# Kernel optimization log

Measured on AMD Instinct MI355X. Metric: run time of the kernel, lower is better.

Reference implementation:

```python
import jax, jax.numpy as jnp
import numpy as np

H = 3        # num heads
K_ = 16      # codebook size per head (k_**H == k == 4096)
D = 768      # full vector dim
DH = D // H  # per-head dim


def setup_inputs() -> dict:
    key = jax.random.key(0)
    kx, kk, ka = jax.random.split(key, 3)
    x = jax.random.normal(kx, (16, 4096, D), dtype=jnp.float32)
    kernel = jax.random.normal(kk, (H, K_, DH), dtype=jnp.float32)
    alpha = jax.random.uniform(ka, (), dtype=jnp.float32)
    return {"x": x, "kernel": kernel, "alpha": alpha}


def reference(x, kernel, alpha):
    B, S, _ = x.shape
    xh = x.reshape(B, S, H, DH)  # split into per-head chunks
    # squared L2 distance [B,S,H,K_]; argmin identical to argmin of tf.norm
    sq = (jnp.sum(xh * xh, axis=-1)[..., None]
          - 2.0 * jnp.einsum('bshd,hkd->bshk', xh, kernel)
          + jnp.sum(kernel * kernel, axis=-1))
    ind = jnp.argmin(sq, axis=-1)              # [B,S,H] int
    v = kernel[jnp.arange(H), ind]             # per-head gather -> [B,S,H,DH]
    v = v.reshape(B, S, D)
    out = alpha * x + (1.0 - alpha) * v        # convex blend
    base = (K_ ** jnp.arange(H)).astype(ind.dtype)  # [1, K_, K_^2]
    code = jnp.sum(ind * base, axis=-1)        # packed code [B,S]
    return out, code
```

## Files before the change

### kernel.cpp

```cpp
#include <hip/hip_runtime.h>


#define NH 3
#define NK 16
#define DHEAD 256
#define DFULL 768
#define TB 4
#define BLK 256

typedef float f2 __attribute__((ext_vector_type(2)));
typedef float f4 __attribute__((ext_vector_type(4)));

__device__ __forceinline__ float dpp_xor1(float x) {
    return __builtin_bit_cast(float, __builtin_amdgcn_mov_dpp(
        __builtin_bit_cast(int, x), 0xB1, 0xF, 0xF, false));
}
__device__ __forceinline__ float dpp_xor2(float x) {
    return __builtin_bit_cast(float, __builtin_amdgcn_mov_dpp(
        __builtin_bit_cast(int, x), 0x4E, 0xF, 0xF, false));
}
__device__ __forceinline__ float swz_xor4(float x) {
    return __builtin_bit_cast(float, __builtin_amdgcn_ds_swizzle(
        __builtin_bit_cast(int, x), 0x101F));
}
__device__ __forceinline__ float swz_xor8(float x) {
    return __builtin_bit_cast(float, __builtin_amdgcn_ds_swizzle(
        __builtin_bit_cast(int, x), 0x201F));
}
__device__ __forceinline__ float swz_xor16(float x) {
    return __builtin_bit_cast(float, __builtin_amdgcn_ds_swizzle(
        __builtin_bit_cast(int, x), 0x401F));
}

__global__ __launch_bounds__(BLK, 4) void rvq_head_kernel(
    const float* __restrict__ x,
    const float* __restrict__ cb,
    const float* __restrict__ alphap,
    float* __restrict__ out,
    float* __restrict__ codef,
    int tok_per_block)
{
    const int h = blockIdx.y;
    __shared__ float lc[NK * DHEAD];
    __shared__ float lps[BLK];
    __shared__ float lcn[NK];

    const int tid  = threadIdx.x;
    const int lane = tid & 63;
    const int wid  = tid >> 6;

    const int t_base = blockIdx.x * tok_per_block;
    const int t_end  = t_base + tok_per_block;
    const int step   = (BLK / 64) * TB;

    const f4* x4 = (const f4*)x;
    f4* out4     = (f4*)out;

    int t0 = t_base + wid * TB;
    f4 xf[TB];
    #pragma unroll
    for (int t = 0; t < TB; ++t)
        xf[t] = x4[(size_t)(t0 + t) * (DFULL / 4) + h * 64 + lane];

    const f4* cb4 = (const f4*)(cb + (size_t)h * NK * DHEAD);
    f4* lc4w = (f4*)lc;
    #pragma unroll
    for (int i = 0; i < 4; ++i) lc4w[tid + i * BLK] = cb4[tid + i * BLK];

    {
        const int r = tid >> 4, dd = (tid & 15) * 16;
        const f4* p = (const f4*)(cb + (size_t)h * NK * DHEAD + r * DHEAD + dd);
        float s = 0.f;
        #pragma unroll
        for (int q = 0; q < 4; ++q) {
            f4 c = p[q];
            s += c.x * c.x + c.y * c.y + c.z * c.z + c.w * c.w;
        }
        lps[tid] = s;
    }
    __syncthreads();
    if (tid < NK) {
        float s = 0.f;
        #pragma unroll
        for (int q = 0; q < 16; ++q) s += lps[tid * 16 + q];
        lcn[tid] = s;
    }
    __syncthreads();

    const int hl = (((lane >> 1) & 1) << 3) | ((lane & 1) << 2)
                 | (((lane >> 2) & 1) << 1) | ((lane >> 3) & 1);
    const float cn_l  = lcn[hl];
    const float alpha = alphap[0];
    const float beta  = 1.0f - alpha;
    const float kscale = (float)(1 << (4 * h));

    const f4* lc4 = (const f4*)lc;

    while (t0 < t_end) {
        const int t1 = t0 + step;

        f4 xn[TB];
        if (t1 < t_end) {
            #pragma unroll
            for (int t = 0; t < TB; ++t)
                xn[t] = x4[(size_t)(t1 + t) * (DFULL / 4) + h * 64 + lane];
        }

        float v[TB][NK];
        #pragma unroll
        for (int j = 0; j < NK; ++j) {
            f4 c = lc4[((j ^ hl) << 6) | lane];
            #pragma unroll
            for (int t = 0; t < TB; ++t) {
                f2 p = (f2){xf[t].x, xf[t].y} * (f2){c.x, c.y};
                p += (f2){xf[t].z, xf[t].w} * (f2){c.z, c.w};
                v[t][j] = p.x + p.y;
            }
        }

        int bi[TB];
        #pragma unroll
        for (int t = 0; t < TB; ++t) {
            #pragma unroll
            for (int j = 0; j < 8; ++j) v[t][j] += dpp_xor2(v[t][j + 8]);
            #pragma unroll
            for (int j = 0; j < 4; ++j) v[t][j] += dpp_xor1(v[t][j + 4]);
            #pragma unroll
            for (int j = 0; j < 2; ++j) v[t][j] += swz_xor4(v[t][j + 2]);
            v[t][0] += swz_xor8(v[t][1]);
            v[t][0] += swz_xor16(v[t][0]);
            v[t][0] += __shfl_xor(v[t][0], 32);

            const float sc = cn_l - 2.0f * v[t][0];
            float m = sc;
            m = fminf(m, dpp_xor1(m));
            m = fminf(m, dpp_xor2(m));
            m = fminf(m, swz_xor4(m));
            m = fminf(m, swz_xor8(m));
            const unsigned long long mask = __ballot(sc == m);
            const int lmin = __builtin_ctzll(mask);
            bi[t] = (((lmin >> 1) & 1) << 3) | ((lmin & 1) << 2)
                  | (((lmin >> 2) & 1) << 1) | ((lmin >> 3) & 1);
        }

        f4 cw[TB];
        #pragma unroll
        for (int t = 0; t < TB; ++t) cw[t] = lc4[(bi[t] << 6) | lane];

        float bif[TB];
        #pragma unroll
        for (int t = 0; t < TB; ++t) {
            f4 o;
            o.x = alpha * xf[t].x + beta * cw[t].x;
            o.y = alpha * xf[t].y + beta * cw[t].y;
            o.z = alpha * xf[t].z + beta * cw[t].z;
            o.w = alpha * xf[t].w + beta * cw[t].w;
            __builtin_nontemporal_store(o, &out4[(size_t)(t0 + t) * (DFULL / 4)
                                                + h * 64 + lane]);
            bif[t] = (float)bi[t] * kscale;
        }

        const float mya = (lane == 0) ? bif[0] : (lane == 1) ? bif[1]
                        : (lane == 2) ? bif[2] : bif[3];
        if (lane < TB) atomicAdd(codef + t0 + lane, mya);

        t0 = t1;
        #pragma unroll
        for (int t = 0; t < TB; ++t) xf[t] = xn[t];
    }
}

extern "C" void kernel_launch(void* const* d_in, const int* in_sizes, int n_in,
                              void* d_out, int out_size, void* d_ws, size_t ws_size,
                              hipStream_t stream) {
    const float* x      = (const float*)d_in[0];
    const float* cb     = (const float*)d_in[1];
    const float* alphap = (const float*)d_in[2];
    const int n_tokens  = in_sizes[0] / DFULL;
    float* out   = (float*)d_out;
    float* codef = out + (size_t)n_tokens * DFULL;

    hipMemsetAsync(codef, 0, (size_t)n_tokens * sizeof(float), stream);

    const int grid_x = 512;
    const int tok_per_block = n_tokens / grid_x;
    dim3 grid(grid_x, NH);
    rvq_head_kernel<<<grid, BLK, 0, stream>>>(x, cb, alphap, out, codef,
                                              tok_per_block);
}
```

Measured before the change: 431.2 us.

## Prefetch x tiles into LDS with async global_load_lds double buffering

Next-tile loads of x now go straight into a per-wave double-buffered LDS region using global_load_lds, with a manual vmcnt wait, instead of being prefetched into registers. Each iteration reads its tile back from LDS. The argmin, codeword gather and blend are fused into one per-token loop, and the nontemporal output store becomes a regular store. The goals are lower register pressure and better overlap of global loads with compute. In exchange the extra 32 KB of LDS per block may reduce resident blocks per CU, and the hand-set vmcnt count only holds while the order in which loads and stores are issued stays the same.

```diff
diff --git a/kernel.cpp b/kernel.cpp
--- a/kernel.cpp
+++ b/kernel.cpp
@@ -7,6 +7,7 @@
 #define DFULL 768
 #define TB 4
 #define BLK 256
+#define NW (BLK / 64)
 
 typedef float f2 __attribute__((ext_vector_type(2)));
 typedef float f4 __attribute__((ext_vector_type(4)));
@@ -30,6 +31,12 @@
 __device__ __forceinline__ float swz_xor16(float x) {
     return __builtin_bit_cast(float, __builtin_amdgcn_ds_swizzle(
         __builtin_bit_cast(int, x), 0x401F));
+}
+
+__device__ __forceinline__ void async_ld16(const float* g, float* l) {
+    __builtin_amdgcn_global_load_lds(
+        (const __attribute__((address_space(1))) unsigned int*)g,
+        (__attribute__((address_space(3))) unsigned int*)l, 16, 0, 0);
 }
 
 __global__ __launch_bounds__(BLK, 4) void rvq_head_kernel(
@@ -42,6 +49,7 @@
 {
     const int h = blockIdx.y;
     __shared__ float lc[NK * DHEAD];
+    __shared__ float xbuf[2][NW][TB][256];
     __shared__ float lps[BLK];
     __shared__ float lcn[NK];
 
@@ -51,16 +59,16 @@
 
     const int t_base = blockIdx.x * tok_per_block;
     const int t_end  = t_base + tok_per_block;
-    const int step   = (BLK / 64) * TB;
+    const int step   = NW * TB;
 
     const f4* x4 = (const f4*)x;
     f4* out4     = (f4*)out;
 
     int t0 = t_base + wid * TB;
-    f4 xf[TB];
     #pragma unroll
     for (int t = 0; t < TB; ++t)
-        xf[t] = x4[(size_t)(t0 + t) * (DFULL / 4) + h * 64 + lane];
+        async_ld16((const float*)&x4[(size_t)(t0 + t) * (DFULL / 4) + h * 64 + lane],
+                   &xbuf[0][wid][t][0]);
 
     const f4* cb4 = (const f4*)(cb + (size_t)h * NK * DHEAD);
     f4* lc4w = (f4*)lc;
@@ -96,15 +104,25 @@
 
     const f4* lc4 = (const f4*)lc;
 
+    int cur = 0;
     while (t0 < t_end) {
         const int t1 = t0 + step;
 
-        f4 xn[TB];
+        asm volatile("s_waitcnt vmcnt(5)" ::: "memory");
+
         if (t1 < t_end) {
             #pragma unroll
             for (int t = 0; t < TB; ++t)
-                xn[t] = x4[(size_t)(t1 + t) * (DFULL / 4) + h * 64 + lane];
-        }
+                async_ld16((const float*)&x4[(size_t)(t1 + t) * (DFULL / 4)
+                                             + h * 64 + lane],
+                           &xbuf[cur ^ 1][wid][t][0]);
+        }
+        asm volatile("" ::: "memory");
+
+        f4 xf[TB];
+        #pragma unroll
+        for (int t = 0; t < TB; ++t)
+            xf[t] = *(const f4*)&xbuf[cur][wid][t][lane * 4];
 
         float v[TB][NK];
         #pragma unroll
@@ -118,7 +136,6 @@
             }
         }
 
-        int bi[TB];
         #pragma unroll
         for (int t = 0; t < TB; ++t) {
             #pragma unroll
@@ -130,7 +147,11 @@
             v[t][0] += swz_xor8(v[t][1]);
             v[t][0] += swz_xor16(v[t][0]);
             v[t][0] += __shfl_xor(v[t][0], 32);
-
+        }
+
+        float bif[TB];
+        #pragma unroll
+        for (int t = 0; t < TB; ++t) {
             const float sc = cn_l - 2.0f * v[t][0];
             float m = sc;
             m = fminf(m, dpp_xor1(m));
@@ -139,25 +160,16 @@
             m = fminf(m, swz_xor8(m));
             const unsigned long long mask = __ballot(sc == m);
             const int lmin = __builtin_ctzll(mask);
-            bi[t] = (((lmin >> 1) & 1) << 3) | ((lmin & 1) << 2)
-                  | (((lmin >> 2) & 1) << 1) | ((lmin >> 3) & 1);
-        }
-
-        f4 cw[TB];
-        #pragma unroll
-        for (int t = 0; t < TB; ++t) cw[t] = lc4[(bi[t] << 6) | lane];
-
-        float bif[TB];
-        #pragma unroll
-        for (int t = 0; t < TB; ++t) {
+            const int bi = (((lmin >> 1) & 1) << 3) | ((lmin & 1) << 2)
+                         | (((lmin >> 2) & 1) << 1) | ((lmin >> 3) & 1);
+            const f4 c = lc4[(bi << 6) | lane];
             f4 o;
-            o.x = alpha * xf[t].x + beta * cw[t].x;
-            o.y = alpha * xf[t].y + beta * cw[t].y;
-            o.z = alpha * xf[t].z + beta * cw[t].z;
-            o.w = alpha * xf[t].w + beta * cw[t].w;
-            __builtin_nontemporal_store(o, &out4[(size_t)(t0 + t) * (DFULL / 4)
-                                                + h * 64 + lane]);
-            bif[t] = (float)bi[t] * kscale;
+            o.x = alpha * xf[t].x + beta * c.x;
+            o.y = alpha * xf[t].y + beta * c.y;
+            o.z = alpha * xf[t].z + beta * c.z;
+            o.w = alpha * xf[t].w + beta * c.w;
+            out4[(size_t)(t0 + t) * (DFULL / 4) + h * 64 + lane] = o;
+            bif[t] = (float)bi * kscale;
         }
 
         const float mya = (lane == 0) ? bif[0] : (lane == 1) ? bif[1]
@@ -165,8 +177,7 @@
         if (lane < TB) atomicAdd(codef + t0 + lane, mya);
 
         t0 = t1;
-        #pragma unroll
-        for (int t = 0; t < TB; ++t) xf[t] = xn[t];
+        cur ^= 1;
     }
 }
 
```

Result: faster. 352.2 us (-18.3%).
